# Optimization experiments

Measured on AMD Instinct MI355X. Metric: run time of the kernel, lower is better.

## Reference

```python
import jax, jax.numpy as jnp
import numpy as np

B, T, C, H = 4, 2048, 1024, 16
D = C // H  # head_dim = 64

def setup_inputs() -> dict:
    key = jax.random.key(0)
    k1, k2, k3 = jax.random.split(key, 3)
    x = jax.random.normal(k1, (B, T, C), dtype=jnp.float32)
    W_attn = jax.random.normal(k2, (C, 3 * C), dtype=jnp.float32) * (C ** -0.5)
    b_attn = jnp.zeros((3 * C,), dtype=jnp.float32)
    W_proj = jax.random.normal(k3, (C, C), dtype=jnp.float32) * (C ** -0.5)
    b_proj = jnp.zeros((C,), dtype=jnp.float32)
    return {"x": x, "W_attn": W_attn, "b_attn": b_attn, "W_proj": W_proj, "b_proj": b_proj}

def reference(x, W_attn, b_attn, W_proj, b_proj):
    Bc, Tc, Cc = x.shape
    qkv = x @ W_attn + b_attn                       # [B,T,3C]
    q, k, v = jnp.split(qkv, 3, axis=-1)
    q = q.reshape(Bc, Tc, H, D).transpose(0, 2, 1, 3)  # [B,H,T,D]
    k = k.reshape(Bc, Tc, H, D).transpose(0, 2, 1, 3)
    v = v.reshape(Bc, Tc, H, D).transpose(0, 2, 1, 3)
    scores = jnp.einsum('bhqd,bhkd->bhqk', q, k) / jnp.sqrt(jnp.float32(D))
    causal = jnp.tril(jnp.ones((Tc, Tc), dtype=bool))
    scores = jnp.where(causal[None, None, :, :], scores, jnp.float32(-jnp.inf))
    wei = jax.nn.softmax(scores, axis=-1)           # dropout=0 -> identity
    out = jnp.einsum('bhqk,bhkd->bhqd', wei, v)     # [B,H,T,D]
    out = out.transpose(0, 2, 1, 3).reshape(Bc, Tc, Cc)
    return out @ W_proj + b_proj
```

## Files before the change

### kernel.cpp

```cpp
#include <hip/hip_runtime.h>
#include <cstdint>
#include <cstddef>

#define Bsz   4
#define Tsz   2048
#define Csz   1024
#define Hn    16
#define Dh    64
#define Mrows 8192
#define KD    1024

#define NEG_BIG (-1.0e30f)
#define SCL2 0.18033688011112042f

typedef unsigned short u16;
typedef __bf16  bf16x8 __attribute__((ext_vector_type(8)));
typedef __bf16  bf16x2 __attribute__((ext_vector_type(2)));
typedef float   f32x4  __attribute__((ext_vector_type(4)));

__device__ __forceinline__ u16 f2bf(float f) {
  union { float f; unsigned int i; } v; v.f = f;
  unsigned int u = v.i;
  return (u16)((u + 0x7fffu + ((u >> 16) & 1u)) >> 16);
}
__device__ __forceinline__ unsigned int pack2bf(float a, float b) {
#if __has_builtin(__builtin_amdgcn_cvt_pk_bf16_f32)
  union { bf16x2 h; unsigned int u; } cv;
  cv.h = __builtin_amdgcn_cvt_pk_bf16_f32(a, b);
  return cv.u;
#else
  return (unsigned int)f2bf(a) | ((unsigned int)f2bf(b) << 16);
#endif
}
__device__ __forceinline__ float fast_exp2(float x) {
#if __has_builtin(__builtin_amdgcn_exp2f)
  return __builtin_amdgcn_exp2f(x);
#else
  return exp2f(x);
#endif
}

__global__ __launch_bounds__(256)
void cvt_f32_bf16(const float* __restrict__ in, u16* __restrict__ out, int n4) {
  const int i = blockIdx.x * 256 + threadIdx.x;
  if (i >= n4) return;
  const float4 v = ((const float4*)in)[i];
  uint2 o;
  o.x = pack2bf(v.x, v.y);
  o.y = pack2bf(v.z, v.w);
  ((uint2*)out)[i] = o;
}

__global__ __launch_bounds__(256)
void transpose_f32_bf16(const float* __restrict__ in, u16* __restrict__ out,
                        int rows, int cols) {
  __shared__ u16 tile[64][65];
  const int tc = blockIdx.x * 64, tr = blockIdx.y * 64;
  const int x = threadIdx.x & 63, y0 = threadIdx.x >> 6;
#pragma unroll
  for (int yy = 0; yy < 64; yy += 4) {
    int r = yy + y0;
    tile[r][x] = f2bf(in[(size_t)(tr + r) * cols + tc + x]);
  }
  __syncthreads();
#pragma unroll
  for (int yy = 0; yy < 64; yy += 4) {
    int r = yy + y0;
    out[(size_t)(tc + r) * rows + tr + x] = tile[x][r];
  }
}

template<int MODE>
__global__ __launch_bounds__(256)
void gemm_bt(const u16* __restrict__ A, const u16* __restrict__ BT,
             const float* __restrict__ bias, u16* __restrict__ o0,
             u16* __restrict__ o1, u16* __restrict__ o2,
             float* __restrict__ fout, int N) {
  __shared__ u16 lsA[128 * 32];
  __shared__ u16 lsB[128 * 32];
  const int tid  = threadIdx.x;
  const int lane = tid & 63;
  const int wid  = tid >> 6;
  const int wm   = wid & 1, wn = wid >> 1;
  const int quad = lane >> 4, l15 = lane & 15;
  const int m0 = blockIdx.y * 128, n0 = blockIdx.x * 128;

  f32x4 acc[4][4];
#pragma unroll
  for (int i = 0; i < 4; ++i)
#pragma unroll
    for (int j = 0; j < 4; ++j) acc[i][j] = (f32x4){0.f, 0.f, 0.f, 0.f};

#if __has_builtin(__builtin_amdgcn_global_load_lds)
  const int srow = lane >> 2, schunk = lane & 3;
  const u16* gA = A  + (size_t)(m0 + wid * 32 + srow) * KD + schunk * 8;
  const u16* gB = BT + (size_t)(n0 + wid * 32 + srow) * KD + schunk * 8;
  u16* lA0 = &lsA[(wid * 32) * 32];
  u16* lB0 = &lsB[(wid * 32) * 32];
#endif

  for (int kk = 0; kk < KD; kk += 32) {
#if __has_builtin(__builtin_amdgcn_global_load_lds)
#pragma unroll
    for (int i = 0; i < 2; ++i) {
      __builtin_amdgcn_global_load_lds(
          (const __attribute__((address_space(1))) void*)(gA + (size_t)i * 16 * KD + kk),
          (__attribute__((address_space(3))) void*)(lA0 + i * 16 * 32), 16, 0, 0);
      __builtin_amdgcn_global_load_lds(
          (const __attribute__((address_space(1))) void*)(gB + (size_t)i * 16 * KD + kk),
          (__attribute__((address_space(3))) void*)(lB0 + i * 16 * 32), 16, 0, 0);
    }
#else
#pragma unroll
    for (int cc = 0; cc < 2; ++cc) {
      int c = tid + cc * 256;
      int row = c >> 2, ch = c & 3;
      *(uint4*)&lsA[row * 32 + ch * 8] =
          *(const uint4*)&A[(size_t)(m0 + row) * KD + kk + ch * 8];
      *(uint4*)&lsB[row * 32 + ch * 8] =
          *(const uint4*)&BT[(size_t)(n0 + row) * KD + kk + ch * 8];
    }
#endif
    __syncthreads();
    bf16x8 af[4], bfv[4];
#pragma unroll
    for (int i = 0; i < 4; ++i)
      af[i] = *(const bf16x8*)&lsA[(wm * 64 + i * 16 + l15) * 32 + quad * 8];
#pragma unroll
    for (int j = 0; j < 4; ++j)
      bfv[j] = *(const bf16x8*)&lsB[(wn * 64 + j * 16 + l15) * 32 + quad * 8];
#pragma unroll
    for (int i = 0; i < 4; ++i)
#pragma unroll
      for (int j = 0; j < 4; ++j)
        acc[i][j] = __builtin_amdgcn_mfma_f32_16x16x32_bf16(af[i], bfv[j],
                                                            acc[i][j], 0, 0, 0);
    __syncthreads();
  }

#pragma unroll
  for (int i = 0; i < 4; ++i) {
#pragma unroll
    for (int j = 0; j < 4; ++j) {
      const int colb = n0 + wn * 64 + j * 16 + l15;
      const float bv = bias[colb];
      float vals[4];
#pragma unroll
      for (int r = 0; r < 4; ++r) vals[r] = acc[i][j][r] + bv;
      const int row0 = m0 + wm * 64 + i * 16 + quad * 4;
      if (MODE == 0) {
        const int b = row0 >> 11, t0 = row0 & (Tsz - 1);
        const int region = colb >> 10;
        const int nc = colb & (Csz - 1);
        const int h = nc >> 6, d = nc & 63;
        if (region == 2) {
          uint2 st;
          st.x = pack2bf(vals[0], vals[1]);
          st.y = pack2bf(vals[2], vals[3]);
          *(uint2*)&o2[((size_t)((b << 4) + h) * Dh + d) * Tsz + t0] = st;
        } else {
          u16* dst = (region == 0) ? o0 : o1;
#pragma unroll
          for (int r = 0; r < 4; ++r)
            dst[(size_t)(((b << 4) + h) * Tsz + t0 + r) * Dh + d] = f2bf(vals[r]);
        }
      } else {
#pragma unroll
        for (int r = 0; r < 4; ++r)
          fout[(size_t)(row0 + r) * N + colb] = vals[r];
      }
    }
  }
}

__global__ __launch_bounds__(256)
void attn_fused(const u16* __restrict__ qb, const u16* __restrict__ kbuf,
                const u16* __restrict__ vT, u16* __restrict__ outp) {
  __shared__ u16 Kl[64 * 72];
  __shared__ u16 Vt[64 * 72];
  const int tid = threadIdx.x, lane = tid & 63, w = tid >> 6;
  const int quad = lane >> 4, l15 = lane & 15;
  const int bh = blockIdx.x;
  const int jq = 31 - blockIdx.y;
  const int b = bh >> 4, h = bh & 15;
  const u16* Q   = qb   + (size_t)bh * Tsz * Dh;
  const u16* Kg  = kbuf + (size_t)bh * Tsz * Dh;
  const u16* VTg = vT   + (size_t)bh * Dh * Tsz;

  const int qrow = jq * 64 + w * 16 + l15;
  const bf16x8 bq0 = *(const bf16x8*)&Q[(size_t)qrow * Dh + quad * 8];
  const bf16x8 bq1 = *(const bf16x8*)&Q[(size_t)qrow * Dh + 32 + quad * 8];

  f32x4 O[4];
#pragma unroll
  for (int nb = 0; nb < 4; ++nb) O[nb] = (f32x4){0.f, 0.f, 0.f, 0.f};
  float m_i = NEG_BIG, l_i = 0.f;

  for (int j = 0; j <= jq; ++j) {
    const int kb = j * 64;
#pragma unroll
    for (int cc = 0; cc < 2; ++cc) {
      const int c = tid + cc * 256;
      const int rr = c >> 3, off = c & 7;
      *(uint4*)&Kl[rr * 72 + off * 8] =
          *(const uint4*)&Kg[(size_t)(kb + rr) * Dh + off * 8];
      *(uint4*)&Vt[rr * 72 + off * 8] =
          *(const uint4*)&VTg[(size_t)rr * Tsz + kb + off * 8];
    }
    __syncthreads();

    const bool diag = (j == jq);
    const int tmax = diag ? (w + 1) : 4;

    f32x4 S[4];
#pragma unroll
    for (int t = 0; t < 4; ++t) S[t] = (f32x4){0.f, 0.f, 0.f, 0.f};
#pragma unroll
    for (int t = 0; t < 4; ++t) {
      if (t < tmax) {
        bf16x8 ak = *(const bf16x8*)&Kl[(t * 16 + l15) * 72 + quad * 8];
        S[t] = __builtin_amdgcn_mfma_f32_16x16x32_bf16(ak, bq0, S[t], 0, 0, 0);
        ak = *(const bf16x8*)&Kl[(t * 16 + l15) * 72 + 32 + quad * 8];
        S[t] = __builtin_amdgcn_mfma_f32_16x16x32_bf16(ak, bq1, S[t], 0, 0, 0);
      }
    }

    float s[4][4];
#pragma unroll
    for (int t = 0; t < 4; ++t)
#pragma unroll
      for (int r = 0; r < 4; ++r) s[t][r] = NEG_BIG;
    if (diag) {
#pragma unroll
      for (int t = 0; t < 4; ++t) {
        if (t < tmax) {
          const int key0 = kb + t * 16 + quad * 4;
#pragma unroll
          for (int r = 0; r < 4; ++r)
            s[t][r] = (key0 + r <= qrow) ? S[t][r] : NEG_BIG;
        }
      }
    } else {
#pragma unroll
      for (int t = 0; t < 4; ++t)
#pragma unroll
        for (int r = 0; r < 4; ++r) s[t][r] = S[t][r];
    }

    float mx = s[0][0];
#pragma unroll
    for (int t = 0; t < 4; ++t)
#pragma unroll
      for (int r = 0; r < 4; ++r) mx = fmaxf(mx, s[t][r]);
    mx = fmaxf(mx, __shfl_xor(mx, 16, 64));
    mx = fmaxf(mx, __shfl_xor(mx, 32, 64));
    const float mn = fmaxf(m_i, mx);
    const float alpha = fast_exp2((m_i - mn) * SCL2);
    float p[4][4], rs = 0.f;
#pragma unroll
    for (int t = 0; t < 4; ++t)
#pragma unroll
      for (int r = 0; r < 4; ++r) {
        p[t][r] = fast_exp2((s[t][r] - mn) * SCL2);
        rs += p[t][r];
      }
    rs += __shfl_xor(rs, 16, 64);
    rs += __shfl_xor(rs, 32, 64);
    l_i = l_i * alpha + rs;
    m_i = mn;

#pragma unroll
    for (int nb = 0; nb < 4; ++nb)
#pragma unroll
      for (int r = 0; r < 4; ++r) O[nb][r] *= alpha;

    union PB { unsigned int u32[4]; bf16x8 v; } pb;
    pb.u32[0] = pack2bf(p[0][0], p[0][1]);
    pb.u32[1] = pack2bf(p[0][2], p[0][3]);
    pb.u32[2] = pack2bf(p[1][0], p[1][1]);
    pb.u32[3] = pack2bf(p[1][2], p[1][3]);
#pragma unroll
    for (int nb = 0; nb < 4; ++nb) {
      union { uint2 d[2]; bf16x8 v; } av;
      av.d[0] = *(const uint2*)&Vt[(nb * 16 + l15) * 72 + quad * 4];
      av.d[1] = *(const uint2*)&Vt[(nb * 16 + l15) * 72 + 16 + quad * 4];
      O[nb] = __builtin_amdgcn_mfma_f32_16x16x32_bf16(av.v, pb.v, O[nb], 0, 0, 0);
    }
    if (tmax > 2) {
      pb.u32[0] = pack2bf(p[2][0], p[2][1]);
      pb.u32[1] = pack2bf(p[2][2], p[2][3]);
      pb.u32[2] = pack2bf(p[3][0], p[3][1]);
      pb.u32[3] = pack2bf(p[3][2], p[3][3]);
#pragma unroll
      for (int nb = 0; nb < 4; ++nb) {
        union { uint2 d[2]; bf16x8 v; } av;
        av.d[0] = *(const uint2*)&Vt[(nb * 16 + l15) * 72 + 32 + quad * 4];
        av.d[1] = *(const uint2*)&Vt[(nb * 16 + l15) * 72 + 48 + quad * 4];
        O[nb] = __builtin_amdgcn_mfma_f32_16x16x32_bf16(av.v, pb.v, O[nb], 0, 0, 0);
      }
    }
    __syncthreads();
  }

  const float inv = 1.0f / l_i;
#pragma unroll
  for (int nb = 0; nb < 4; ++nb) {
    uint2 st;
    st.x = pack2bf(O[nb][0] * inv, O[nb][1] * inv);
    st.y = pack2bf(O[nb][2] * inv, O[nb][3] * inv);
    *(uint2*)&outp[(size_t)(b * Tsz + qrow) * Csz + h * Dh + nb * 16 + quad * 4] = st;
  }
}

extern "C" void kernel_launch(void* const* d_in, const int* in_sizes, int n_in,
                              void* d_out, int out_size, void* d_ws, size_t ws_size,
                              hipStream_t stream) {
  const float* x      = (const float*)d_in[0];
  const float* W_attn = (const float*)d_in[1];
  const float* b_attn = (const float*)d_in[2];
  const float* W_proj = (const float*)d_in[3];
  const float* b_proj = (const float*)d_in[4];
  float* out = (float*)d_out;

  u16* ws   = (u16*)d_ws;
  u16* xbf  = ws;
  u16* qbuf = xbf  + (size_t)Mrows * Csz;
  u16* kbuf = qbuf + (size_t)Mrows * Csz;
  u16* vbuf = kbuf + (size_t)Mrows * Csz;
  u16* aout = vbuf + (size_t)Mrows * Csz;
  u16* WTa  = aout + (size_t)Mrows * Csz;
  u16* WTp  = WTa  + (size_t)Csz * 3 * Csz;

  cvt_f32_bf16<<<(Mrows * Csz / 4 + 255) / 256, 256, 0, stream>>>(
      x, xbf, Mrows * Csz / 4);
  transpose_f32_bf16<<<dim3(3 * Csz / 64, Csz / 64), 256, 0, stream>>>(
      W_attn, WTa, Csz, 3 * Csz);
  transpose_f32_bf16<<<dim3(Csz / 64, Csz / 64), 256, 0, stream>>>(
      W_proj, WTp, Csz, Csz);
  gemm_bt<0><<<dim3(3 * Csz / 128, Mrows / 128), 256, 0, stream>>>(
      xbf, WTa, b_attn, qbuf, kbuf, vbuf, nullptr, 3 * Csz);
  attn_fused<<<dim3(Bsz * Hn, Tsz / 64), 256, 0, stream>>>(
      qbuf, kbuf, vbuf, aout);
  gemm_bt<1><<<dim3(Csz / 128, Mrows / 128), 256, 0, stream>>>(
      aout, WTp, b_proj, nullptr, nullptr, nullptr, out, Csz);
}
```

Measured before the change: 273.4 us.

## Pair complementary causal query blocks per workgroup to balance work and reuse K/V tiles

Each workgroup now processes two query blocks, jq=31-y and jq=y, which together always span 33 key tiles. This balances causal work across blocks and halves the grid. Each K/V tile loaded into LDS serves both query blocks, which cuts global K/V traffic. The cost is higher register pressure from two sets of accumulators and Q fragments, and fewer workgroups (64x16) to hide latency.

```diff
diff --git a/kernel.cpp b/kernel.cpp
--- a/kernel.cpp
+++ b/kernel.cpp
@@ -181,23 +181,118 @@
   const int tid = threadIdx.x, lane = tid & 63, w = tid >> 6;
   const int quad = lane >> 4, l15 = lane & 15;
   const int bh = blockIdx.x;
-  const int jq = 31 - blockIdx.y;
+  const int jqA = 31 - blockIdx.y;
+  const int jqB = blockIdx.y;
   const int b = bh >> 4, h = bh & 15;
   const u16* Q   = qb   + (size_t)bh * Tsz * Dh;
   const u16* Kg  = kbuf + (size_t)bh * Tsz * Dh;
   const u16* VTg = vT   + (size_t)bh * Dh * Tsz;
 
-  const int qrow = jq * 64 + w * 16 + l15;
-  const bf16x8 bq0 = *(const bf16x8*)&Q[(size_t)qrow * Dh + quad * 8];
-  const bf16x8 bq1 = *(const bf16x8*)&Q[(size_t)qrow * Dh + 32 + quad * 8];
-
-  f32x4 O[4];
-#pragma unroll
-  for (int nb = 0; nb < 4; ++nb) O[nb] = (f32x4){0.f, 0.f, 0.f, 0.f};
-  float m_i = NEG_BIG, l_i = 0.f;
-
-  for (int j = 0; j <= jq; ++j) {
-    const int kb = j * 64;
+  const int qrowA = jqA * 64 + w * 16 + l15;
+  const int qrowB = jqB * 64 + w * 16 + l15;
+  const bf16x8 aqA0 = *(const bf16x8*)&Q[(size_t)qrowA * Dh + quad * 8];
+  const bf16x8 aqA1 = *(const bf16x8*)&Q[(size_t)qrowA * Dh + 32 + quad * 8];
+  const bf16x8 aqB0 = *(const bf16x8*)&Q[(size_t)qrowB * Dh + quad * 8];
+  const bf16x8 aqB1 = *(const bf16x8*)&Q[(size_t)qrowB * Dh + 32 + quad * 8];
+
+  f32x4 OA[4], OB[4];
+#pragma unroll
+  for (int nb = 0; nb < 4; ++nb) {
+    OA[nb] = (f32x4){0.f, 0.f, 0.f, 0.f};
+    OB[nb] = (f32x4){0.f, 0.f, 0.f, 0.f};
+  }
+  float mA = NEG_BIG, lA = 0.f, mB = NEG_BIG, lB = 0.f;
+
+  int kb = 0;
+
+  auto tile_update = [&](const bf16x8& bq0, const bf16x8& bq1, f32x4* O,
+                         float& m_i, float& l_i, int qrow, bool diag) {
+    const int tmax = diag ? (w + 1) : 4;
+    f32x4 S[4];
+#pragma unroll
+    for (int t = 0; t < 4; ++t) S[t] = (f32x4){0.f, 0.f, 0.f, 0.f};
+#pragma unroll
+    for (int t = 0; t < 4; ++t) {
+      if (t < tmax) {
+        bf16x8 ak = *(const bf16x8*)&Kl[(t * 16 + l15) * 72 + quad * 8];
+        S[t] = __builtin_amdgcn_mfma_f32_16x16x32_bf16(ak, bq0, S[t], 0, 0, 0);
+        ak = *(const bf16x8*)&Kl[(t * 16 + l15) * 72 + 32 + quad * 8];
+        S[t] = __builtin_amdgcn_mfma_f32_16x16x32_bf16(ak, bq1, S[t], 0, 0, 0);
+      }
+    }
+
+    float s[4][4];
+    if (diag) {
+#pragma unroll
+      for (int t = 0; t < 4; ++t) {
+        const int key0 = kb + t * 16 + quad * 4;
+#pragma unroll
+        for (int r = 0; r < 4; ++r)
+          s[t][r] = (t < tmax && key0 + r <= qrow) ? S[t][r] : NEG_BIG;
+      }
+    } else {
+#pragma unroll
+      for (int t = 0; t < 4; ++t)
+#pragma unroll
+        for (int r = 0; r < 4; ++r) s[t][r] = S[t][r];
+    }
+
+    float mx = s[0][0];
+#pragma unroll
+    for (int t = 0; t < 4; ++t)
+#pragma unroll
+      for (int r = 0; r < 4; ++r) mx = fmaxf(mx, s[t][r]);
+    mx = fmaxf(mx, __shfl_xor(mx, 16, 64));
+    mx = fmaxf(mx, __shfl_xor(mx, 32, 64));
+    const float mn = fmaxf(m_i, mx);
+    const float alpha = fast_exp2((m_i - mn) * SCL2);
+    float p[4][4], rs = 0.f;
+#pragma unroll
+    for (int t = 0; t < 4; ++t)
+#pragma unroll
+      for (int r = 0; r < 4; ++r) {
+        p[t][r] = fast_exp2((s[t][r] - mn) * SCL2);
+        rs += p[t][r];
+      }
+    rs += __shfl_xor(rs, 16, 64);
+    rs += __shfl_xor(rs, 32, 64);
+    l_i = l_i * alpha + rs;
+    m_i = mn;
+
+#pragma unroll
+    for (int nb = 0; nb < 4; ++nb)
+#pragma unroll
+      for (int r = 0; r < 4; ++r) O[nb][r] *= alpha;
+
+    union PB { unsigned int u32[4]; bf16x8 v; } pb;
+    pb.u32[0] = pack2bf(p[0][0], p[0][1]);
+    pb.u32[1] = pack2bf(p[0][2], p[0][3]);
+    pb.u32[2] = pack2bf(p[1][0], p[1][1]);
+    pb.u32[3] = pack2bf(p[1][2], p[1][3]);
+#pragma unroll
+    for (int nb = 0; nb < 4; ++nb) {
+      union { uint2 d[2]; bf16x8 v; } av;
+      av.d[0] = *(const uint2*)&Vt[(nb * 16 + l15) * 72 + quad * 4];
+      av.d[1] = *(const uint2*)&Vt[(nb * 16 + l15) * 72 + 16 + quad * 4];
+      O[nb] = __builtin_amdgcn_mfma_f32_16x16x32_bf16(av.v, pb.v, O[nb], 0, 0, 0);
+    }
+    if (tmax > 2) {
+      pb.u32[0] = pack2bf(p[2][0], p[2][1]);
+      pb.u32[1] = pack2bf(p[2][2], p[2][3]);
+      pb.u32[2] = pack2bf(p[3][0], p[3][1]);
+      pb.u32[3] = pack2bf(p[3][2], p[3][3]);
+#pragma unroll
+      for (int nb = 0; nb < 4; ++nb) {
+        union { uint2 d[2]; bf16x8 v; } av;
+        av.d[0] = *(const uint2*)&Vt[(nb * 16 + l15) * 72 + 32 + quad * 4];
+        av.d[1] = *(const uint2*)&Vt[(nb * 16 + l15) * 72 + 48 + quad * 4];
+        O[nb] = __builtin_amdgcn_mfma_f32_16x16x32_bf16(av.v, pb.v, O[nb], 0, 0, 0);
+      }
+    }
+  };
+
+  for (int j = 0; j <= jqA; ++j) {
+    kb = j * 64;
 #pragma unroll
     for (int cc = 0; cc < 2; ++cc) {
       const int c = tid + cc * 256;
@@ -209,106 +304,22 @@
     }
     __syncthreads();
 
-    const bool diag = (j == jq);
-    const int tmax = diag ? (w + 1) : 4;
-
-    f32x4 S[4];
-#pragma unroll
-    for (int t = 0; t < 4; ++t) S[t] = (f32x4){0.f, 0.f, 0.f, 0.f};
-#pragma unroll
-    for (int t = 0; t < 4; ++t) {
-      if (t < tmax) {
-        bf16x8 ak = *(const bf16x8*)&Kl[(t * 16 + l15) * 72 + quad * 8];
-        S[t] = __builtin_amdgcn_mfma_f32_16x16x32_bf16(ak, bq0, S[t], 0, 0, 0);
-        ak = *(const bf16x8*)&Kl[(t * 16 + l15) * 72 + 32 + quad * 8];
-        S[t] = __builtin_amdgcn_mfma_f32_16x16x32_bf16(ak, bq1, S[t], 0, 0, 0);
-      }
-    }
-
-    float s[4][4];
-#pragma unroll
-    for (int t = 0; t < 4; ++t)
-#pragma unroll
-      for (int r = 0; r < 4; ++r) s[t][r] = NEG_BIG;
-    if (diag) {
-#pragma unroll
-      for (int t = 0; t < 4; ++t) {
-        if (t < tmax) {
-          const int key0 = kb + t * 16 + quad * 4;
-#pragma unroll
-          for (int r = 0; r < 4; ++r)
-            s[t][r] = (key0 + r <= qrow) ? S[t][r] : NEG_BIG;
-        }
-      }
-    } else {
-#pragma unroll
-      for (int t = 0; t < 4; ++t)
-#pragma unroll
-        for (int r = 0; r < 4; ++r) s[t][r] = S[t][r];
-    }
-
-    float mx = s[0][0];
-#pragma unroll
-    for (int t = 0; t < 4; ++t)
-#pragma unroll
-      for (int r = 0; r < 4; ++r) mx = fmaxf(mx, s[t][r]);
-    mx = fmaxf(mx, __shfl_xor(mx, 16, 64));
-    mx = fmaxf(mx, __shfl_xor(mx, 32, 64));
-    const float mn = fmaxf(m_i, mx);
-    const float alpha = fast_exp2((m_i - mn) * SCL2);
-    float p[4][4], rs = 0.f;
-#pragma unroll
-    for (int t = 0; t < 4; ++t)
-#pragma unroll
-      for (int r = 0; r < 4; ++r) {
-        p[t][r] = fast_exp2((s[t][r] - mn) * SCL2);
-        rs += p[t][r];
-      }
-    rs += __shfl_xor(rs, 16, 64);
-    rs += __shfl_xor(rs, 32, 64);
-    l_i = l_i * alpha + rs;
-    m_i = mn;
-
-#pragma unroll
-    for (int nb = 0; nb < 4; ++nb)
-#pragma unroll
-      for (int r = 0; r < 4; ++r) O[nb][r] *= alpha;
-
-    union PB { unsigned int u32[4]; bf16x8 v; } pb;
-    pb.u32[0] = pack2bf(p[0][0], p[0][1]);
-    pb.u32[1] = pack2bf(p[0][2], p[0][3]);
-    pb.u32[2] = pack2bf(p[1][0], p[1][1]);
-    pb.u32[3] = pack2bf(p[1][2], p[1][3]);
-#pragma unroll
-    for (int nb = 0; nb < 4; ++nb) {
-      union { uint2 d[2]; bf16x8 v; } av;
-      av.d[0] = *(const uint2*)&Vt[(nb * 16 + l15) * 72 + quad * 4];
-      av.d[1] = *(const uint2*)&Vt[(nb * 16 + l15) * 72 + 16 + quad * 4];
-      O[nb] = __builtin_amdgcn_mfma_f32_16x16x32_bf16(av.v, pb.v, O[nb], 0, 0, 0);
-    }
-    if (tmax > 2) {
-      pb.u32[0] = pack2bf(p[2][0], p[2][1]);
-      pb.u32[1] = pack2bf(p[2][2], p[2][3]);
-      pb.u32[2] = pack2bf(p[3][0], p[3][1]);
-      pb.u32[3] = pack2bf(p[3][2], p[3][3]);
-#pragma unroll
-      for (int nb = 0; nb < 4; ++nb) {
-        union { uint2 d[2]; bf16x8 v; } av;
-        av.d[0] = *(const uint2*)&Vt[(nb * 16 + l15) * 72 + 32 + quad * 4];
-        av.d[1] = *(const uint2*)&Vt[(nb * 16 + l15) * 72 + 48 + quad * 4];
-        O[nb] = __builtin_amdgcn_mfma_f32_16x16x32_bf16(av.v, pb.v, O[nb], 0, 0, 0);
-      }
-    }
+    tile_update(aqA0, aqA1, OA, mA, lA, qrowA, j == jqA);
+    if (j <= jqB) tile_update(aqB0, aqB1, OB, mB, lB, qrowB, j == jqB);
+
     __syncthreads();
   }
 
-  const float inv = 1.0f / l_i;
+  const float invA = 1.0f / lA, invB = 1.0f / lB;
 #pragma unroll
   for (int nb = 0; nb < 4; ++nb) {
     uint2 st;
-    st.x = pack2bf(O[nb][0] * inv, O[nb][1] * inv);
-    st.y = pack2bf(O[nb][2] * inv, O[nb][3] * inv);
-    *(uint2*)&outp[(size_t)(b * Tsz + qrow) * Csz + h * Dh + nb * 16 + quad * 4] = st;
+    st.x = pack2bf(OA[nb][0] * invA, OA[nb][1] * invA);
+    st.y = pack2bf(OA[nb][2] * invA, OA[nb][3] * invA);
+    *(uint2*)&outp[(size_t)(b * Tsz + qrowA) * Csz + h * Dh + nb * 16 + quad * 4] = st;
+    st.x = pack2bf(OB[nb][0] * invB, OB[nb][1] * invB);
+    st.y = pack2bf(OB[nb][2] * invB, OB[nb][3] * invB);
+    *(uint2*)&outp[(size_t)(b * Tsz + qrowB) * Csz + h * Dh + nb * 16 + quad * 4] = st;
   }
 }
 
@@ -339,7 +350,7 @@
       W_proj, WTp, Csz, Csz);
   gemm_bt<0><<<dim3(3 * Csz / 128, Mrows / 128), 256, 0, stream>>>(
       xbf, WTa, b_attn, qbuf, kbuf, vbuf, nullptr, 3 * Csz);
-  attn_fused<<<dim3(Bsz * Hn, Tsz / 64), 256, 0, stream>>>(
+  attn_fused<<<dim3(Bsz * Hn, Tsz / 128), 256, 0, stream>>>(
       qbuf, kbuf, vbuf, aout);
   gemm_bt<1><<<dim3(Csz / 128, Mrows / 128), 256, 0, stream>>>(
       aout, WTp, b_proj, nullptr, nullptr, nullptr, out, Csz);
```

Measured after the change: 286.4 us. 4.8% more time.
